# Kernel optimization log

Hardware: AMD Instinct MI355X
Metric: run time of the kernel (lower is better)

## Reference

```python
import jax, jax.numpy as jnp
import numpy as np

B, D, L, E, H = 8192, 1024, 256, 16, 400

def setup_inputs() -> dict:
    key = jax.random.key(0)
    ks = jax.random.split(key, 6)
    s1 = 1.0 / np.sqrt(D)
    s2 = 1.0 / np.sqrt(H)
    return {
        "x": jax.random.normal(ks[0], (B, D), dtype=jnp.float32),
        "angle_idx": jax.random.randint(ks[1], (B,), 0, E, dtype=jnp.int64),
        "W1": jax.random.uniform(ks[2], (E, D, H), jnp.float32, -s1, s1),
        "b1": jax.random.uniform(ks[3], (E, H), jnp.float32, -s1, s1),
        "W2": jax.random.uniform(ks[4], (E, H, 2 * L), jnp.float32, -s2, s2),
        "b2": jax.random.uniform(ks[5], (E, 2 * L), jnp.float32, -s2, s2),
    }

def reference(x, angle_idx, W1, b1, W2, b2):
    # Dense all-experts compute, then per-sample select (jit-friendly MoE dispatch).
    # h1: [E, B, H]
    h1 = jax.nn.relu(jnp.einsum('bd,edh->ebh', x, W1) + b1[:, None, :])
    # h: [E, B, 2L]
    h = jnp.einsum('ebh,ehk->ebk', h1, W2) + b2[:, None, :]
    sel = h[angle_idx, jnp.arange(x.shape[0])]  # [B, 2L], each row from its routed expert
    half = sel.shape[1] // 2
    z_mu, z_logvar = sel[:, :half], sel[:, half:]
    return (z_mu, z_logvar)
```

## Files before the change

kernel.cpp:

```cpp
#include <hip/hip_runtime.h>
#include <hip/hip_bf16.h>
#include <cstdint>
#include <cstddef>

#define B_N 8192
#define D_K 1024
#define H_N 400
#define HP  416
#define K2_N 512
#define E_N 16
#define L_N 256
#define TM 64
#define PAD_ROWS (B_N + E_N * TM)
#define NTILES (PAD_ROWS / TM)

typedef short bf16x8 __attribute__((ext_vector_type(8)));
typedef float f32x4 __attribute__((ext_vector_type(4)));

#define GLDS(gp, lp) __builtin_amdgcn_global_load_lds( \
    (const __attribute__((address_space(1))) unsigned int*)(gp), \
    (__attribute__((address_space(3))) unsigned int*)(lp), 16, 0, 0)

static __device__ __forceinline__ unsigned short f2bf(float f) {
  union { float f; unsigned int u; } c; c.f = f;
  unsigned int u = c.u + 0x7fffu + ((c.u >> 16) & 1u);
  return (unsigned short)(u >> 16);
}
static __device__ __forceinline__ unsigned int pkbf(float a, float b) {
  union { __hip_bfloat162 v; unsigned int u; } c;
  c.v = __float22bfloat162_rn(make_float2(a, b));
  return c.u;
}

__global__ __launch_bounds__(256) void hist_kernel(const int* __restrict__ idx,
                                                   int* __restrict__ hist) {
  __shared__ int h[E_N];
  const int t = threadIdx.x;
  if (t < E_N) h[t] = 0;
  __syncthreads();
  atomicAdd(&h[idx[blockIdx.x * 256 + t]], 1);
  __syncthreads();
  if (t < E_N) hist[blockIdx.x * E_N + t] = h[t];
}

__global__ __launch_bounds__(256) void prep_kernel(const float* __restrict__ W1,
                                                   const float* __restrict__ W2,
                                                   const float* __restrict__ x,
                                                   const int* __restrict__ idx,
                                                   const int* __restrict__ hist,
                                                   unsigned short* __restrict__ Wt1,
                                                   unsigned short* __restrict__ Wt2,
                                                   unsigned short* __restrict__ xc,
                                                   int* __restrict__ off_al,
                                                   int* __restrict__ cnt_al,
                                                   int* __restrict__ order) {
  const int bid = blockIdx.x;
  const int t = threadIdx.x;
  if (bid < 2688) {
    __shared__ unsigned short Ls[64][72];
    const float* S; unsigned short* Dt; int K, N, Kd, Nd, k0, n0;
    if (bid < 1792) {
      int e = bid / 112, r = bid % 112;
      k0 = (r % 16) * 64; n0 = (r / 16) * 64;
      S = W1 + (size_t)e * D_K * H_N; Dt = Wt1 + (size_t)e * HP * D_K;
      K = D_K; N = H_N; Kd = D_K; Nd = HP;
    } else {
      int t2 = bid - 1792; int e = t2 / 56, r = t2 % 56;
      k0 = (r % 7) * 64; n0 = (r / 7) * 64;
      S = W2 + (size_t)e * H_N * K2_N; Dt = Wt2 + (size_t)e * K2_N * HP;
      K = H_N; N = K2_N; Kd = HP; Nd = K2_N;
    }
    const int kk = t >> 4;
    const int nn = (t & 15) * 4;
    float4 v[4];
#pragma unroll
    for (int p = 0; p < 4; ++p) {
      int k = k0 + p * 16 + kk;
      int n = n0 + nn;
      v[p] = make_float4(0.f, 0.f, 0.f, 0.f);
      if (k < K && n + 3 < N) v[p] = *(const float4*)(S + (size_t)k * N + n);
    }
#pragma unroll
    for (int p = 0; p < 4; ++p) {
      Ls[nn + 0][p * 16 + kk] = f2bf(v[p].x);
      Ls[nn + 1][p * 16 + kk] = f2bf(v[p].y);
      Ls[nn + 2][p * 16 + kk] = f2bf(v[p].z);
      Ls[nn + 3][p * 16 + kk] = f2bf(v[p].w);
    }
    __syncthreads();
    const int n2 = t >> 3;
    const int ch = t & 7;
#pragma unroll
    for (int p = 0; p < 2; ++p) {
      int n = n0 + p * 32 + n2;
      int k = k0 + ch * 8;
      if (n < Nd && k < Kd)
        *(uint4*)(Dt + (size_t)n * Kd + k) = *(const uint4*)&Ls[p * 32 + n2][ch * 8];
    }
  } else if (bid < 3200) {
    const int xb = bid - 2688;
    const float* S = x + (size_t)xb * 16 * D_K;
    unsigned short* Dp = xc + (size_t)xb * 16 * D_K;
#pragma unroll
    for (int i = 0; i < 16; ++i) {
      float4 v = *(const float4*)(S + i * D_K + t * 4);
      uint2 o; o.x = pkbf(v.x, v.y); o.y = pkbf(v.z, v.w);
      *(uint2*)(Dp + i * D_K + t * 4) = o;
    }
  } else {
    const int hb = bid - 3200;
    __shared__ int totL[E_N], preL[E_N], offsL[E_N], curL[E_N];
    if (t < E_N) {
      int pre = 0, tot = 0;
      for (int b = 0; b < 32; ++b) {
        int h = hist[b * E_N + t];
        if (b < hb) pre += h;
        tot += h;
      }
      totL[t] = tot; preL[t] = pre;
    }
    __syncthreads();
    if (t == 0) {
      int acc = 0;
      for (int e = 0; e < E_N; ++e) {
        offsL[e] = acc;
        if (hb == 0) off_al[e] = acc;
        acc += ((totL[e] + TM - 1) / TM) * TM;
      }
      if (hb == 0) off_al[E_N] = acc;
    }
    __syncthreads();
    if (t < E_N) {
      curL[t] = offsL[t] + preL[t];
      if (hb == 0) cnt_al[t] = totL[t];
    }
    __syncthreads();
    const int b = hb * 256 + t;
    const int e = idx[b];
    const int slot = atomicAdd(&curL[e], 1);
    order[slot] = b;
    if (hb == 0) *(uint2*)(xc + (size_t)B_N * D_K + t * 4) = make_uint2(0, 0);
  }
}

__global__ __launch_bounds__(256) void gemm1_kernel(const unsigned short* __restrict__ xc,
                                                    const unsigned short* __restrict__ Wt1,
                                                    const float* __restrict__ b1,
                                                    const int* __restrict__ off_al,
                                                    const int* __restrict__ cnt_al,
                                                    const int* __restrict__ order,
                                                    unsigned short* __restrict__ h1buf) {
  __shared__ unsigned short As[2 * 2 * 2048];
  __shared__ unsigned short Bs[2 * 2 * 4096];
  __shared__ int offs[E_N + 1];
  __shared__ int rowidx[TM];
  const int tid = threadIdx.x;
  const int m0 = blockIdx.x * TM;
  const int nb = blockIdx.y;
  if (tid <= E_N) offs[tid] = off_al[tid];
  __syncthreads();
  if (m0 >= offs[E_N]) return;
  int e = 0;
  while (m0 >= offs[e + 1]) ++e;
  if (tid < TM) {
    const bool valid = (m0 + tid) < (offs[e] + cnt_al[e]);
    rowidx[tid] = valid ? order[m0 + tid] : B_N;
  }
  __syncthreads();
  const unsigned short* Wt1e = Wt1 + (size_t)e * HP * D_K;

  const int l = tid & 63, w = tid >> 6;
  const int r4 = l >> 2;
  const int sg = (r4 ^ (r4 >> 2)) & 3;
  const int g8 = ((l & 3) ^ sg) * 8;
  const int t0 = nb * 8 + 2 * w;
  const bool act0 = (t0 < 25);
  const bool act1 = (t0 + 1 < 25);
  const unsigned short* gA = xc + (size_t)rowidx[16 * w + r4] * D_K + g8;
  const unsigned short* gB0 = Wt1e + (size_t)(t0 * 16 + r4) * D_K + g8;
  const unsigned short* gB1 = gB0 + (size_t)16 * D_K;

  const int ln = l & 15, q = l >> 4;
  const int sr = (ln ^ (ln >> 2)) & 3;
  const int cq = (q ^ sr) * 8;

  f32x4 acc[4][2] = {};

#pragma unroll
  for (int ks = 0; ks < 2; ++ks) {
    GLDS(gA + ks * 32, &As[ks * 2048 + 16 * w * 32]);
    if (act0) GLDS(gB0 + ks * 32, &Bs[ks * 4096 + (2 * w + 0) * 512]);
    if (act1) GLDS(gB1 + ks * 32, &Bs[ks * 4096 + (2 * w + 1) * 512]);
  }

  for (int k0 = 0; k0 < D_K; k0 += 64) {
    const int cur = (k0 >> 6) & 1;
    const int nxt = cur ^ 1;
    __syncthreads();
    if (k0 + 64 < D_K) {
#pragma unroll
      for (int ks = 0; ks < 2; ++ks) {
        const int kg = k0 + 64 + ks * 32;
        GLDS(gA + kg, &As[nxt * 4096 + ks * 2048 + 16 * w * 32]);
        if (act0) GLDS(gB0 + kg, &Bs[nxt * 8192 + ks * 4096 + (2 * w + 0) * 512]);
        if (act1) GLDS(gB1 + kg, &Bs[nxt * 8192 + ks * 4096 + (2 * w + 1) * 512]);
      }
    }
    if (act0) {
#pragma unroll
      for (int ks = 0; ks < 2; ++ks) {
        const unsigned short* Ab = &As[cur * 4096 + ks * 2048];
        const unsigned short* Bb = &Bs[cur * 8192 + ks * 4096];
        bf16x8 af[4];
#pragma unroll
        for (int i = 0; i < 4; ++i)
          af[i] = *(const bf16x8*)&Ab[(16 * i + ln) * 32 + cq];
        bf16x8 b0f = *(const bf16x8*)&Bb[(2 * w + 0) * 512 + ln * 32 + cq];
#pragma unroll
        for (int i = 0; i < 4; ++i)
          acc[i][0] = __builtin_amdgcn_mfma_f32_16x16x32_bf16(b0f, af[i], acc[i][0], 0, 0, 0);
        if (act1) {
          bf16x8 b1f = *(const bf16x8*)&Bb[(2 * w + 1) * 512 + ln * 32 + cq];
#pragma unroll
          for (int i = 0; i < 4; ++i)
            acc[i][1] = __builtin_amdgcn_mfma_f32_16x16x32_bf16(b1f, af[i], acc[i][1], 0, 0, 0);
        }
      }
    }
  }

#pragma unroll
  for (int j = 0; j < 2; ++j) {
    if (j == 0 ? act0 : act1) {
      const int n4 = (t0 + j) * 16 + 4 * q;
      const float4 bv = *(const float4*)&b1[e * H_N + n4];
#pragma unroll
      for (int i = 0; i < 4; ++i) {
        const size_t m = (size_t)(m0 + 16 * i + ln);
        uint2 o;
        o.x = pkbf(fmaxf(acc[i][j][0] + bv.x, 0.f), fmaxf(acc[i][j][1] + bv.y, 0.f));
        o.y = pkbf(fmaxf(acc[i][j][2] + bv.z, 0.f), fmaxf(acc[i][j][3] + bv.w, 0.f));
        *(uint2*)&h1buf[m * HP + n4] = o;
      }
    }
  }
}

__global__ __launch_bounds__(256) void gemm2_kernel(const unsigned short* __restrict__ h1buf,
                                                    const unsigned short* __restrict__ Wt2,
                                                    const float* __restrict__ b2,
                                                    const int* __restrict__ off_al,
                                                    const int* __restrict__ cnt_al,
                                                    const int* __restrict__ order,
                                                    float* __restrict__ out) {
  __shared__ unsigned short As[2 * 2 * 2048];
  __shared__ unsigned short Bs[2 * 2 * 4096];
  __shared__ int offs[E_N + 1];
  __shared__ int rowidx[TM];
  const int tid = threadIdx.x;
  const int m0 = blockIdx.x * TM;
  const int nb = blockIdx.y;
  if (tid <= E_N) offs[tid] = off_al[tid];
  __syncthreads();
  if (m0 >= offs[E_N]) return;
  int e = 0;
  while (m0 >= offs[e + 1]) ++e;
  if (tid < TM) {
    const bool valid = (m0 + tid) < (offs[e] + cnt_al[e]);
    rowidx[tid] = valid ? order[m0 + tid] : -1;
  }
  __syncthreads();
  const unsigned short* Wt2e = Wt2 + (size_t)e * K2_N * HP;

  const int l = tid & 63, w = tid >> 6;
  const int r4 = l >> 2;
  const int sg = (r4 ^ (r4 >> 2)) & 3;
  const int g8 = ((l & 3) ^ sg) * 8;
  const int t0 = nb * 8 + 2 * w;
  const unsigned short* gA = h1buf + (size_t)(m0 + 16 * w + r4) * HP + g8;
  const unsigned short* gB0 = Wt2e + (size_t)(t0 * 16 + r4) * HP + g8;
  const unsigned short* gB1 = gB0 + (size_t)16 * HP;

  const int ln = l & 15, q = l >> 4;
  const int sr = (ln ^ (ln >> 2)) & 3;
  const int cq = (q ^ sr) * 8;

  f32x4 acc[4][2] = {};

#pragma unroll
  for (int ks = 0; ks < 2; ++ks) {
    GLDS(gA + ks * 32, &As[ks * 2048 + 16 * w * 32]);
    GLDS(gB0 + ks * 32, &Bs[ks * 4096 + (2 * w + 0) * 512]);
    GLDS(gB1 + ks * 32, &Bs[ks * 4096 + (2 * w + 1) * 512]);
  }

  for (int k0 = 0; k0 < HP; k0 += 64) {
    const int cur = (k0 >> 6) & 1;
    const int nxt = cur ^ 1;
    __syncthreads();
#pragma unroll
    for (int ks = 0; ks < 2; ++ks) {
      const int kg = k0 + 64 + ks * 32;
      if (kg < HP) {
        GLDS(gA + kg, &As[nxt * 4096 + ks * 2048 + 16 * w * 32]);
        GLDS(gB0 + kg, &Bs[nxt * 8192 + ks * 4096 + (2 * w + 0) * 512]);
        GLDS(gB1 + kg, &Bs[nxt * 8192 + ks * 4096 + (2 * w + 1) * 512]);
      }
    }
#pragma unroll
    for (int ks = 0; ks < 2; ++ks) {
      if (k0 + ks * 32 < HP) {
        const unsigned short* Ab = &As[cur * 4096 + ks * 2048];
        const unsigned short* Bb = &Bs[cur * 8192 + ks * 4096];
        bf16x8 af[4];
#pragma unroll
        for (int i = 0; i < 4; ++i)
          af[i] = *(const bf16x8*)&Ab[(16 * i + ln) * 32 + cq];
        bf16x8 b0f = *(const bf16x8*)&Bb[(2 * w + 0) * 512 + ln * 32 + cq];
#pragma unroll
        for (int i = 0; i < 4; ++i)
          acc[i][0] = __builtin_amdgcn_mfma_f32_16x16x32_bf16(b0f, af[i], acc[i][0], 0, 0, 0);
        bf16x8 b1f = *(const bf16x8*)&Bb[(2 * w + 1) * 512 + ln * 32 + cq];
#pragma unroll
        for (int i = 0; i < 4; ++i)
          acc[i][1] = __builtin_amdgcn_mfma_f32_16x16x32_bf16(b1f, af[i], acc[i][1], 0, 0, 0);
      }
    }
  }

#pragma unroll
  for (int j = 0; j < 2; ++j) {
    const int n4 = (t0 + j) * 16 + 4 * q;
    const float4 bv = *(const float4*)&b2[e * K2_N + n4];
#pragma unroll
    for (int i = 0; i < 4; ++i) {
      const int s = rowidx[16 * i + ln];
      if (s >= 0) {
        float4 v;
        v.x = acc[i][j][0] + bv.x;
        v.y = acc[i][j][1] + bv.y;
        v.z = acc[i][j][2] + bv.z;
        v.w = acc[i][j][3] + bv.w;
        if (n4 < L_N) *(float4*)&out[(size_t)s * L_N + n4] = v;
        else          *(float4*)&out[(size_t)(B_N + s) * L_N + (n4 - L_N)] = v;
      }
    }
  }
}

extern "C" void kernel_launch(void* const* d_in, const int* in_sizes, int n_in,
                              void* d_out, int out_size, void* d_ws, size_t ws_size,
                              hipStream_t stream) {
  const float* x   = (const float*)d_in[0];
  const int*   idx = (const int*)d_in[1];
  const float* W1  = (const float*)d_in[2];
  const float* b1  = (const float*)d_in[3];
  const float* W2  = (const float*)d_in[4];
  const float* b2  = (const float*)d_in[5];
  float* out = (float*)d_out;

  char* ws = (char*)d_ws;
  int* off_al = (int*)(ws + 0);
  int* cnt_al = (int*)(ws + 128);
  int* hist   = (int*)(ws + 192);
  int* order  = (int*)(ws + 2240);
  unsigned short* xc  = (unsigned short*)(ws + 39104);
  unsigned short* h1  = (unsigned short*)(ws + 16818368);
  unsigned short* Wt1 = (unsigned short*)(ws + 24486080);
  unsigned short* Wt2 = (unsigned short*)(ws + 38117568);

  hist_kernel<<<32, 256, 0, stream>>>(idx, hist);
  prep_kernel<<<3232, 256, 0, stream>>>(W1, W2, x, idx, hist, Wt1, Wt2, xc,
                                        off_al, cnt_al, order);
  gemm1_kernel<<<dim3(NTILES, 4), 256, 0, stream>>>(xc, Wt1, b1, off_al, cnt_al, order, h1);
  gemm2_kernel<<<dim3(NTILES, 4), 256, 0, stream>>>(h1, Wt2, b2, off_al, cnt_al, order, out);
}
```

Before: 163.9 us.

## Fold expert histogram into prep kernel and swizzle GEMM blocks per XCD

Removes the separate histogram launch by having each routing block in the prep kernel recount all expert indices with shared-memory atomics. Both GEMM kernels now remap block ids so that blocks landing on the same XCD process contiguous M tiles and N blocks, improving L2 reuse of expert weights and activations. The cost is redundant index scanning across 32 blocks and a fixed swizzle tied to the grid size.

```diff
diff --git a/kernel.cpp b/kernel.cpp
--- a/kernel.cpp
+++ b/kernel.cpp
@@ -32,22 +32,10 @@
   return c.u;
 }
 
-__global__ __launch_bounds__(256) void hist_kernel(const int* __restrict__ idx,
-                                                   int* __restrict__ hist) {
-  __shared__ int h[E_N];
-  const int t = threadIdx.x;
-  if (t < E_N) h[t] = 0;
-  __syncthreads();
-  atomicAdd(&h[idx[blockIdx.x * 256 + t]], 1);
-  __syncthreads();
-  if (t < E_N) hist[blockIdx.x * E_N + t] = h[t];
-}
-
 __global__ __launch_bounds__(256) void prep_kernel(const float* __restrict__ W1,
                                                    const float* __restrict__ W2,
                                                    const float* __restrict__ x,
                                                    const int* __restrict__ idx,
-                                                   const int* __restrict__ hist,
                                                    unsigned short* __restrict__ Wt1,
                                                    unsigned short* __restrict__ Wt2,
                                                    unsigned short* __restrict__ xc,
@@ -110,14 +98,13 @@
   } else {
     const int hb = bid - 3200;
     __shared__ int totL[E_N], preL[E_N], offsL[E_N], curL[E_N];
-    if (t < E_N) {
-      int pre = 0, tot = 0;
-      for (int b = 0; b < 32; ++b) {
-        int h = hist[b * E_N + t];
-        if (b < hb) pre += h;
-        tot += h;
-      }
-      totL[t] = tot; preL[t] = pre;
+    if (t < E_N) { totL[t] = 0; preL[t] = 0; }
+    __syncthreads();
+    const int lim = hb * 256;
+    for (int i = t; i < B_N; i += 256) {
+      const int e0 = idx[i];
+      atomicAdd(&totL[e0], 1);
+      if (i < lim) atomicAdd(&preL[e0], 1);
     }
     __syncthreads();
     if (t == 0) {
@@ -141,6 +128,13 @@
     order[slot] = b;
     if (hb == 0) *(uint2*)(xc + (size_t)B_N * D_K + t * 4) = make_uint2(0, 0);
   }
+}
+
+static __device__ __forceinline__ void swz_decode(int bx, int by, int& mt, int& nb) {
+  const int L = bx + NTILES * by;
+  const int vid = (L & 7) * 72 + (L >> 3);
+  mt = vid >> 2;
+  nb = vid & 3;
 }
 
 __global__ __launch_bounds__(256) void gemm1_kernel(const unsigned short* __restrict__ xc,
@@ -155,8 +149,9 @@
   __shared__ int offs[E_N + 1];
   __shared__ int rowidx[TM];
   const int tid = threadIdx.x;
-  const int m0 = blockIdx.x * TM;
-  const int nb = blockIdx.y;
+  int mt, nb;
+  swz_decode(blockIdx.x, blockIdx.y, mt, nb);
+  const int m0 = mt * TM;
   if (tid <= E_N) offs[tid] = off_al[tid];
   __syncthreads();
   if (m0 >= offs[E_N]) return;
@@ -258,8 +253,9 @@
   __shared__ int offs[E_N + 1];
   __shared__ int rowidx[TM];
   const int tid = threadIdx.x;
-  const int m0 = blockIdx.x * TM;
-  const int nb = blockIdx.y;
+  int mt, nb;
+  swz_decode(blockIdx.x, blockIdx.y, mt, nb);
+  const int m0 = mt * TM;
   if (tid <= E_N) offs[tid] = off_al[tid];
   __syncthreads();
   if (m0 >= offs[E_N]) return;
@@ -362,15 +358,13 @@
   char* ws = (char*)d_ws;
   int* off_al = (int*)(ws + 0);
   int* cnt_al = (int*)(ws + 128);
-  int* hist   = (int*)(ws + 192);
   int* order  = (int*)(ws + 2240);
   unsigned short* xc  = (unsigned short*)(ws + 39104);
   unsigned short* h1  = (unsigned short*)(ws + 16818368);
   unsigned short* Wt1 = (unsigned short*)(ws + 24486080);
   unsigned short* Wt2 = (unsigned short*)(ws + 38117568);
 
-  hist_kernel<<<32, 256, 0, stream>>>(idx, hist);
-  prep_kernel<<<3232, 256, 0, stream>>>(W1, W2, x, idx, hist, Wt1, Wt2, xc,
+  prep_kernel<<<3232, 256, 0, stream>>>(W1, W2, x, idx, Wt1, Wt2, xc,
                                         off_al, cnt_al, order);
   gemm1_kernel<<<dim3(NTILES, 4), 256, 0, stream>>>(xc, Wt1, b1, off_al, cnt_al, order, h1);
   gemm2_kernel<<<dim3(NTILES, 4), 256, 0, stream>>>(h1, Wt2, b2, off_al, cnt_al, order, out);
```

Measured after the change: 159.5 us. 2.7% less time.
